# Optimization experiments

Hardware: AMD Instinct MI355X
Metric: run time of the kernel (lower is better)

Reference implementation:

```python
import jax, jax.numpy as jnp
import numpy as np

D_MODEL = 512
NUM_HEADS = 8
D_K = D_MODEL // NUM_HEADS
DIM_FF = 2048
EPS = 1e-5


def layer_norm(x, gamma, beta):
    mu = jnp.mean(x, axis=-1, keepdims=True)
    var = jnp.mean(jnp.square(x - mu), axis=-1, keepdims=True)
    return (x - mu) * jax.lax.rsqrt(var + EPS) * gamma + beta


def setup_inputs() -> dict:
    key = jax.random.key(0)
    ks = jax.random.split(key, 10)
    B, L = 8, 1024
    s = 1.0 / np.sqrt(D_MODEL)
    return {
        "h": jax.random.normal(ks[0], (B, L, D_MODEL), jnp.float32),
        "attn_bias": jax.random.normal(ks[1], (B, NUM_HEADS, L, L), jnp.float32),
        "mask": jnp.ones((B, L), jnp.int32),
        "Wqkv": jax.random.normal(ks[2], (D_MODEL, 3 * D_MODEL), jnp.float32) * s,
        "bqkv": jnp.zeros((3 * D_MODEL,), jnp.float32),
        "Wo": jax.random.normal(ks[3], (D_MODEL, D_MODEL), jnp.float32) * s,
        "bo": jnp.zeros((D_MODEL,), jnp.float32),
        "W1": jax.random.normal(ks[4], (D_MODEL, DIM_FF), jnp.float32) * s,
        "b1": jnp.zeros((DIM_FF,), jnp.float32),
        "W2": jax.random.normal(ks[5], (DIM_FF, D_MODEL), jnp.float32) * (1.0 / np.sqrt(DIM_FF)),
        "b2": jnp.zeros((D_MODEL,), jnp.float32),
        "g1": jnp.ones((D_MODEL,), jnp.float32),
        "be1": jnp.zeros((D_MODEL,), jnp.float32),
        "g2": jnp.ones((D_MODEL,), jnp.float32),
        "be2": jnp.zeros((D_MODEL,), jnp.float32),
    }


def reference(h, attn_bias, mask, Wqkv, bqkv, Wo, bo, W1, b1, W2, b2, g1, be1, g2, be2):
    B, L, D = h.shape
    H, dk = NUM_HEADS, D_K
    qkv = h @ Wqkv + bqkv                      # [B, L, 3D]
    q, k, v = jnp.split(qkv, 3, axis=-1)
    q = q.reshape(B, L, H, dk).transpose(0, 2, 1, 3)  # [B, H, L, dk]
    k = k.reshape(B, L, H, dk).transpose(0, 2, 1, 3)
    v = v.reshape(B, L, H, dk).transpose(0, 2, 1, 3)
    scores = jnp.einsum('bhqd,bhkd->bhqk', q, k) / np.sqrt(dk)
    scores = scores + attn_bias
    scores = jnp.where(mask[:, None, None, :] > 0, scores, -jnp.inf)
    attn = jax.nn.softmax(scores, axis=-1)
    out = jnp.einsum('bhqk,bhkd->bhqd', attn, v)       # [B, H, L, dk]
    out = out.transpose(0, 2, 1, 3).reshape(B, L, D)
    out = out @ Wo + bo
    h = layer_norm(h + out, g1, be1)
    ff = jax.nn.relu(h @ W1 + b1) @ W2 + b2
    h = layer_norm(h + ff, g2, be2)
    return h
```

## Files before the change

kernel.cpp:

```cpp
#include <hip/hip_runtime.h>
#include <hip/hip_bf16.h>
#include <math.h>

#define NUM_HEADS 8
#define SEQ_L 1024
#define EPS 1e-5f
#define LOG2E 1.44269504088896f

typedef __bf16 bf16x8 __attribute__((ext_vector_type(8)));
typedef float f32x4 __attribute__((ext_vector_type(4)));
typedef __hip_bfloat16 bf16;

#define AS1 __attribute__((address_space(1)))
#define AS3 __attribute__((address_space(3)))

__device__ __forceinline__ void gload_lds16(const void* g, void* l) {
    __builtin_amdgcn_global_load_lds((const AS1 unsigned*)g, (AS3 unsigned*)l, 16, 0, 0);
}

__device__ __forceinline__ unsigned short bfb(float x) {
    bf16 b = __float2bfloat16(x);
    return *(unsigned short*)&b;
}

__device__ __forceinline__ int swz(int el, int row) { return el ^ ((row & 7) << 3); }

__global__ __launch_bounds__(256) void prep_kernel(
    const float* __restrict__ h, const float* __restrict__ Wqkv,
    const float* __restrict__ Wo, const float* __restrict__ W1,
    const float* __restrict__ W2,
    bf16* __restrict__ hb, bf16* __restrict__ Wtq, bf16* __restrict__ Wto,
    bf16* __restrict__ Wt1, bf16* __restrict__ Wt2)
{
    const int bid = blockIdx.x;
    const int tid = threadIdx.x;
    if (bid < 2048) {
        const int i = (bid * 256 + tid) * 8;
        const float4 v0 = *(const float4*)&h[i];
        const float4 v1 = *(const float4*)&h[i + 4];
        uint4 w;
        w.x = (unsigned)bfb(v0.x) | ((unsigned)bfb(v0.y) << 16);
        w.y = (unsigned)bfb(v0.z) | ((unsigned)bfb(v0.w) << 16);
        w.z = (unsigned)bfb(v1.x) | ((unsigned)bfb(v1.y) << 16);
        w.w = (unsigned)bfb(v1.z) | ((unsigned)bfb(v1.w) << 16);
        *(uint4*)&hb[i] = w;
        return;
    }
    int r = bid - 2048;
    const float* W; bf16* Wt; int K, N, bx, by;
    if (r < 768)        { W = Wqkv; Wt = Wtq; K = 512;  N = 1536; bx = r % 48; by = r / 48; }
    else if (r < 1024)  { r -= 768;  W = Wo; Wt = Wto; K = 512;  N = 512;  bx = r % 16; by = r / 16; }
    else if (r < 2048)  { r -= 1024; W = W1; Wt = Wt1; K = 512;  N = 2048; bx = r % 64; by = r / 64; }
    else                { r -= 2048; W = W2; Wt = Wt2; K = 2048; N = 512;  bx = r % 16; by = r / 16; }

    __shared__ float t[32][33];
    const int tx = tid & 31, ty = tid >> 5;
    const int n0 = bx * 32, k0 = by * 32;
    #pragma unroll
    for (int q = 0; q < 4; ++q)
        t[ty + 8 * q][tx] = W[(size_t)(k0 + ty + 8 * q) * N + n0 + tx];
    __syncthreads();
    #pragma unroll
    for (int q = 0; q < 4; ++q)
        Wt[(size_t)(n0 + ty + 8 * q) * K + k0 + tx] = __float2bfloat16(t[tx][ty + 8 * q]);
}

__global__ __launch_bounds__(256) void gemm_bf16(
    const bf16* __restrict__ A, const bf16* __restrict__ Bt,
    const float* __restrict__ bias, bf16* __restrict__ Cb,
    int M, int N, int K, int relu)
{
    __shared__ __align__(16) bf16 Abuf[128 * 32];
    __shared__ __align__(16) bf16 Bbuf[128 * 32];
    const int tid = threadIdx.x;
    const int wv = tid >> 6, lane = tid & 63;
    const int row0 = blockIdx.y * 128, col0 = blockIdx.x * 128;
    const int wm = (wv >> 1) * 64, wn = (wv & 1) * 64;
    const int r0 = lane & 15, kb = lane >> 4;

    f32x4 acc[4][4] = {};
    const int arow = lane >> 2;
    const int akoff = (lane & 3) * 8;

    for (int k0 = 0; k0 < K; k0 += 32) {
        #pragma unroll
        for (int s = 0; s < 2; ++s) {
            const int c = 2 * wv + s;
            gload_lds16(&A[(size_t)(row0 + c * 16 + arow) * K + k0 + akoff], &Abuf[c * 512]);
            gload_lds16(&Bt[(size_t)(col0 + c * 16 + arow) * K + k0 + akoff], &Bbuf[c * 512]);
        }
        __syncthreads();

        bf16x8 a[4], b[4];
        #pragma unroll
        for (int i = 0; i < 4; ++i)
            a[i] = *(const bf16x8*)&Abuf[(wm + i * 16 + r0) * 32 + kb * 8];
        #pragma unroll
        for (int j = 0; j < 4; ++j)
            b[j] = *(const bf16x8*)&Bbuf[(wn + j * 16 + r0) * 32 + kb * 8];
        #pragma unroll
        for (int i = 0; i < 4; ++i)
            #pragma unroll
            for (int j = 0; j < 4; ++j)
                acc[i][j] = __builtin_amdgcn_mfma_f32_16x16x32_bf16(a[i], b[j], acc[i][j], 0, 0, 0);
        __syncthreads();
    }

    float bv[4];
    #pragma unroll
    for (int j = 0; j < 4; ++j) bv[j] = bias[col0 + wn + j * 16 + r0];

    #pragma unroll
    for (int i = 0; i < 4; ++i) {
        #pragma unroll
        for (int j = 0; j < 4; ++j) {
            const int col = col0 + wn + j * 16 + r0;
            #pragma unroll
            for (int reg = 0; reg < 4; ++reg) {
                const int row = row0 + wm + i * 16 + kb * 4 + reg;
                float v = acc[i][j][reg] + bv[j];
                if (relu) v = fmaxf(v, 0.f);
                Cb[(size_t)row * N + col] = __float2bfloat16(v);
            }
        }
    }
}

__global__ __launch_bounds__(256) void gemm_qkv(
    const bf16* __restrict__ A, const bf16* __restrict__ Bt,
    const float* __restrict__ bias,
    bf16* __restrict__ Qb, bf16* __restrict__ Kb, bf16* __restrict__ Vtb,
    int M, int N, int K)
{
    __shared__ __align__(16) bf16 Abuf[128 * 32];
    __shared__ __align__(16) bf16 Bbuf[128 * 32];
    const int tid = threadIdx.x;
    const int wv = tid >> 6, lane = tid & 63;
    const int row0 = blockIdx.y * 128, col0 = blockIdx.x * 128;
    const int wm = (wv >> 1) * 64, wn = (wv & 1) * 64;
    const int r0 = lane & 15, kb = lane >> 4;

    f32x4 acc[4][4] = {};
    const int arow = lane >> 2;
    const int akoff = (lane & 3) * 8;

    for (int k0 = 0; k0 < K; k0 += 32) {
        #pragma unroll
        for (int s = 0; s < 2; ++s) {
            const int c = 2 * wv + s;
            gload_lds16(&A[(size_t)(row0 + c * 16 + arow) * K + k0 + akoff], &Abuf[c * 512]);
            gload_lds16(&Bt[(size_t)(col0 + c * 16 + arow) * K + k0 + akoff], &Bbuf[c * 512]);
        }
        __syncthreads();

        bf16x8 a[4], b[4];
        #pragma unroll
        for (int i = 0; i < 4; ++i)
            a[i] = *(const bf16x8*)&Abuf[(wm + i * 16 + r0) * 32 + kb * 8];
        #pragma unroll
        for (int j = 0; j < 4; ++j)
            b[j] = *(const bf16x8*)&Bbuf[(wn + j * 16 + r0) * 32 + kb * 8];
        #pragma unroll
        for (int i = 0; i < 4; ++i)
            #pragma unroll
            for (int j = 0; j < 4; ++j)
                acc[i][j] = __builtin_amdgcn_mfma_f32_16x16x32_bf16(a[i], b[j], acc[i][j], 0, 0, 0);
        __syncthreads();
    }

    #pragma unroll
    for (int i = 0; i < 4; ++i) {
        #pragma unroll
        for (int j = 0; j < 4; ++j) {
            const int col = col0 + wn + j * 16 + r0;
            const float bv = bias[col];
            const int region = col >> 9;
            const int cc = col & 511;
            const int head = cc >> 6, d = cc & 63;
            const int l0 = row0 + wm + i * 16 + kb * 4;
            const int b_ = l0 >> 10, l_ = l0 & 1023;
            if (region == 2) {
                unsigned short pk[4];
                #pragma unroll
                for (int reg = 0; reg < 4; ++reg) pk[reg] = bfb(acc[i][j][reg] + bv);
                *(ushort4*)&Vtb[((size_t)(b_ * NUM_HEADS + head) * 64 + d) * SEQ_L + l_] =
                    make_ushort4(pk[0], pk[1], pk[2], pk[3]);
            } else {
                const float s = (region == 0) ? (0.125f * LOG2E) : 1.0f;
                bf16* dst = (region == 0) ? Qb : Kb;
                #pragma unroll
                for (int reg = 0; reg < 4; ++reg) {
                    dst[((size_t)(b_ * NUM_HEADS + head) * SEQ_L + l_ + reg) * 64 + d] =
                        __float2bfloat16((acc[i][j][reg] + bv) * s);
                }
            }
        }
    }
}

#define KVB 128
__global__ __launch_bounds__(256) void attn_mfma(
    const bf16* __restrict__ Qb, const bf16* __restrict__ Kb,
    const bf16* __restrict__ Vtb, const float* __restrict__ abias,
    const int* __restrict__ mask, bf16* __restrict__ out)
{
    const int bh = blockIdx.y;
    const int b = bh >> 3, h = bh & 7;
    const int q0 = blockIdx.x * 64;
    const int tid = threadIdx.x;
    const int wv = tid >> 6, lane = tid & 63;
    const int ql = lane & 15;
    const int hi = lane >> 4;

    __shared__ __align__(16) bf16 Ks[KVB * 64];
    __shared__ __align__(16) bf16 Vs[64 * KVB];
    __shared__ __align__(16) bf16 Ps[4][16 * KVB];

    const int qrow = q0 + wv * 16 + ql;
    bf16x8 qf[2];
    #pragma unroll
    for (int kk = 0; kk < 2; ++kk)
        qf[kk] = *(const bf16x8*)&Qb[((size_t)bh * SEQ_L + qrow) * 64 + kk * 32 + hi * 8];

    const int skr = tid >> 3;
    const int skc = (tid & 7) * 8;
    const int svr = tid >> 4;
    const int svc = (tid & 15) * 8;

    f32x4 o[4] = {};
    float m = -1e30f, l = 0.f;
    const size_t bias_row = ((size_t)(b * NUM_HEADS + h) * SEQ_L + qrow) * SEQ_L;
    const bf16* Kbase = Kb + (size_t)bh * SEQ_L * 64;
    const bf16* Vbase = Vtb + (size_t)bh * 64 * SEQ_L;
    const int* mbase = mask + b * SEQ_L;

    for (int k0 = 0; k0 < SEQ_L; k0 += KVB) {
        __syncthreads();
        #pragma unroll
        for (int it = 0; it < 4; ++it) {
            const int row = skr + it * 32;
            *(bf16x8*)&Ks[swz(row * 64 + skc, row)] =
                *(const bf16x8*)&Kbase[(size_t)(k0 + row) * 64 + skc];
        }
        #pragma unroll
        for (int it = 0; it < 4; ++it) {
            const int row = svr + it * 16;
            *(bf16x8*)&Vs[swz(row * KVB + svc, row)] =
                *(const bf16x8*)&Vbase[(size_t)row * SEQ_L + k0 + svc];
        }
        __syncthreads();

        f32x4 p[8];
        #pragma unroll
        for (int c = 0; c < 8; ++c) {
            const f32x4 b4 = *(const f32x4*)&abias[bias_row + k0 + c * 16 + hi * 4];
            const int4 m4 = *(const int4*)&mbase[k0 + c * 16 + hi * 4];
            p[c][0] = (m4.x > 0) ? b4[0] * LOG2E : -1e30f;
            p[c][1] = (m4.y > 0) ? b4[1] * LOG2E : -1e30f;
            p[c][2] = (m4.z > 0) ? b4[2] * LOG2E : -1e30f;
            p[c][3] = (m4.w > 0) ? b4[3] * LOG2E : -1e30f;
        }

        __builtin_amdgcn_s_setprio(1);
        #pragma unroll
        for (int c = 0; c < 8; ++c) {
            const int row = c * 16 + ql;
            #pragma unroll
            for (int kk = 0; kk < 2; ++kk) {
                const bf16x8 kf = *(const bf16x8*)&Ks[swz(row * 64 + kk * 32 + hi * 8, row)];
                p[c] = __builtin_amdgcn_mfma_f32_16x16x32_bf16(kf, qf[kk], p[c], 0, 0, 0);
            }
        }
        __builtin_amdgcn_s_setprio(0);

        float mx = p[0][0];
        #pragma unroll
        for (int c = 0; c < 8; ++c)
            #pragma unroll
            for (int reg = 0; reg < 4; ++reg) mx = fmaxf(mx, p[c][reg]);
        mx = fmaxf(mx, __shfl_xor(mx, 16, 64));
        mx = fmaxf(mx, __shfl_xor(mx, 32, 64));

        if (!__all(mx <= m + 11.0f)) {
            const float mnew = fmaxf(m, mx);
            const float scale = __builtin_exp2f(m - mnew);
            m = mnew;
            l *= scale;
            #pragma unroll
            for (int reg = 0; reg < 4; ++reg) {
                const float sc_q = __shfl(scale, (lane & 48) | (hi * 4 + reg), 64);
                #pragma unroll
                for (int c2 = 0; c2 < 4; ++c2) o[c2][reg] *= sc_q;
            }
        }

        float lsum = 0.f;
        #pragma unroll
        for (int c = 0; c < 8; ++c)
            #pragma unroll
            for (int reg = 0; reg < 4; ++reg) {
                const float pv = __builtin_exp2f(p[c][reg] - m);
                p[c][reg] = pv;
                lsum += pv;
            }
        l += lsum;

        #pragma unroll
        for (int c = 0; c < 8; ++c) {
            const int el = ql * KVB + c * 16 + hi * 4;
            uint2 pk;
            pk.x = (unsigned)bfb(p[c][0]) | ((unsigned)bfb(p[c][1]) << 16);
            pk.y = (unsigned)bfb(p[c][2]) | ((unsigned)bfb(p[c][3]) << 16);
            *(uint2*)&Ps[wv][swz(el, ql)] = pk;
        }

        __builtin_amdgcn_s_setprio(1);
        #pragma unroll
        for (int kk = 0; kk < 4; ++kk) {
            const bf16x8 pf = *(const bf16x8*)&Ps[wv][swz(ql * KVB + kk * 32 + hi * 8, ql)];
            #pragma unroll
            for (int c2 = 0; c2 < 4; ++c2) {
                const int vrow = c2 * 16 + ql;
                const bf16x8 vf = *(const bf16x8*)&Vs[swz(vrow * KVB + kk * 32 + hi * 8, vrow)];
                o[c2] = __builtin_amdgcn_mfma_f32_16x16x32_bf16(pf, vf, o[c2], 0, 0, 0);
            }
        }
        __builtin_amdgcn_s_setprio(0);
    }

    l += __shfl_xor(l, 16, 64);
    l += __shfl_xor(l, 32, 64);
    const float invl = (l > 0.f) ? (1.0f / l) : 0.f;
    #pragma unroll
    for (int reg = 0; reg < 4; ++reg) {
        const float inv_q = __shfl(invl, (lane & 48) | (hi * 4 + reg), 64);
        const int row = q0 + wv * 16 + hi * 4 + reg;
        #pragma unroll
        for (int c2 = 0; c2 < 4; ++c2)
            out[((size_t)(b * SEQ_L + row)) * 512 + h * 64 + c2 * 16 + ql] =
                __float2bfloat16(o[c2][reg] * inv_q);
    }
}

__global__ __launch_bounds__(256) void add_ln_to_bf16(
    const float* __restrict__ X, const bf16* __restrict__ Yb,
    const float* __restrict__ gamma, const float* __restrict__ beta,
    bf16* __restrict__ outb)
{
    const int wave = threadIdx.x >> 6;
    const int lane = threadIdx.x & 63;
    const int row = blockIdx.x * 4 + wave;
    const float* xp = X + (size_t)row * 512 + lane * 8;
    const bf16x8 yv = *(const bf16x8*)&Yb[(size_t)row * 512 + lane * 8];

    float v[8];
    const float4 a0 = *(const float4*)xp;
    const float4 a1 = *(const float4*)(xp + 4);
    v[0] = a0.x + (float)yv[0]; v[1] = a0.y + (float)yv[1];
    v[2] = a0.z + (float)yv[2]; v[3] = a0.w + (float)yv[3];
    v[4] = a1.x + (float)yv[4]; v[5] = a1.y + (float)yv[5];
    v[6] = a1.z + (float)yv[6]; v[7] = a1.w + (float)yv[7];

    float s = 0.f, sq = 0.f;
    #pragma unroll
    for (int i = 0; i < 8; ++i) { s += v[i]; sq += v[i] * v[i]; }
    #pragma unroll
    for (int off = 1; off < 64; off <<= 1) {
        s += __shfl_xor(s, off, 64);
        sq += __shfl_xor(sq, off, 64);
    }
    const float mu = s * (1.f / 512.f);
    const float var = sq * (1.f / 512.f) - mu * mu;
    const float rstd = rsqrtf(var + EPS);

    const int c = lane * 8;
    const float4 g0 = *(const float4*)&gamma[c];
    const float4 g1 = *(const float4*)&gamma[c + 4];
    const float4 e0 = *(const float4*)&beta[c];
    const float4 e1 = *(const float4*)&beta[c + 4];
    float r[8];
    r[0] = (v[0] - mu) * rstd * g0.x + e0.x;
    r[1] = (v[1] - mu) * rstd * g0.y + e0.y;
    r[2] = (v[2] - mu) * rstd * g0.z + e0.z;
    r[3] = (v[3] - mu) * rstd * g0.w + e0.w;
    r[4] = (v[4] - mu) * rstd * g1.x + e1.x;
    r[5] = (v[5] - mu) * rstd * g1.y + e1.y;
    r[6] = (v[6] - mu) * rstd * g1.z + e1.z;
    r[7] = (v[7] - mu) * rstd * g1.w + e1.w;

    uint4 w;
    w.x = (unsigned)bfb(r[0]) | ((unsigned)bfb(r[1]) << 16);
    w.y = (unsigned)bfb(r[2]) | ((unsigned)bfb(r[3]) << 16);
    w.z = (unsigned)bfb(r[4]) | ((unsigned)bfb(r[5]) << 16);
    w.w = (unsigned)bfb(r[6]) | ((unsigned)bfb(r[7]) << 16);
    *(uint4*)&outb[(size_t)row * 512 + c] = w;
}

__global__ __launch_bounds__(256) void add_ln_from_bf16(
    const bf16* __restrict__ Xb, const bf16* __restrict__ Yb,
    const float* __restrict__ gamma, const float* __restrict__ beta,
    float* __restrict__ out)
{
    const int wave = threadIdx.x >> 6;
    const int lane = threadIdx.x & 63;
    const int row = blockIdx.x * 4 + wave;
    const bf16x8 xv = *(const bf16x8*)&Xb[(size_t)row * 512 + lane * 8];
    const bf16x8 yv = *(const bf16x8*)&Yb[(size_t)row * 512 + lane * 8];

    float v[8];
    #pragma unroll
    for (int i = 0; i < 8; ++i) v[i] = (float)xv[i] + (float)yv[i];

    float s = 0.f, sq = 0.f;
    #pragma unroll
    for (int i = 0; i < 8; ++i) { s += v[i]; sq += v[i] * v[i]; }
    #pragma unroll
    for (int off = 1; off < 64; off <<= 1) {
        s += __shfl_xor(s, off, 64);
        sq += __shfl_xor(sq, off, 64);
    }
    const float mu = s * (1.f / 512.f);
    const float var = sq * (1.f / 512.f) - mu * mu;
    const float rstd = rsqrtf(var + EPS);

    const int c = lane * 8;
    const float4 g0 = *(const float4*)&gamma[c];
    const float4 g1 = *(const float4*)&gamma[c + 4];
    const float4 e0 = *(const float4*)&beta[c];
    const float4 e1 = *(const float4*)&beta[c + 4];
    float4 r0, r1;
    r0.x = (v[0] - mu) * rstd * g0.x + e0.x;
    r0.y = (v[1] - mu) * rstd * g0.y + e0.y;
    r0.z = (v[2] - mu) * rstd * g0.z + e0.z;
    r0.w = (v[3] - mu) * rstd * g0.w + e0.w;
    r1.x = (v[4] - mu) * rstd * g1.x + e1.x;
    r1.y = (v[5] - mu) * rstd * g1.y + e1.y;
    r1.z = (v[6] - mu) * rstd * g1.z + e1.z;
    r1.w = (v[7] - mu) * rstd * g1.w + e1.w;
    float* op = out + (size_t)row * 512 + c;
    *(float4*)op = r0;
    *(float4*)(op + 4) = r1;
}

extern "C" void kernel_launch(void* const* d_in, const int* in_sizes, int n_in,
                              void* d_out, int out_size, void* d_ws, size_t ws_size,
                              hipStream_t stream)
{
    const float* h    = (const float*)d_in[0];
    const float* ab   = (const float*)d_in[1];
    const int*   mask = (const int*)d_in[2];
    const float* Wqkv = (const float*)d_in[3];
    const float* bqkv = (const float*)d_in[4];
    const float* Wo   = (const float*)d_in[5];
    const float* bo   = (const float*)d_in[6];
    const float* W1   = (const float*)d_in[7];
    const float* b1   = (const float*)d_in[8];
    const float* W2   = (const float*)d_in[9];
    const float* b2   = (const float*)d_in[10];
    const float* g1   = (const float*)d_in[11];
    const float* be1  = (const float*)d_in[12];
    const float* g2   = (const float*)d_in[13];
    const float* be2  = (const float*)d_in[14];
    float* out = (float*)d_out;
    char* ws = (char*)d_ws;

    const int M = 8 * 1024;
    const size_t MB = 1024 * 1024;

    bf16*  hb    = (bf16*)(ws + 0 * MB);
    bf16*  Wtq   = (bf16*)(ws + 8 * MB);
    bf16*  Wto   = (bf16*)(ws + 10 * MB);
    bf16*  Wt1   = (bf16*)(ws + 11 * MB);
    bf16*  Wt2   = (bf16*)(ws + 13 * MB);
    bf16*  Qb    = (bf16*)(ws + 15 * MB);
    bf16*  Kb    = (bf16*)(ws + 23 * MB);
    bf16*  Vtb   = (bf16*)(ws + 31 * MB);
    bf16*  aob   = (bf16*)(ws + 39 * MB);
    bf16*  projb = (bf16*)(ws + 47 * MB);
    bf16*  h1b   = (bf16*)(ws + 55 * MB);
    bf16*  ffb   = (bf16*)(ws + 63 * MB);
    bf16*  f2b   = (bf16*)(ws + 95 * MB);

    prep_kernel<<<dim3(5120), 256, 0, stream>>>(h, Wqkv, Wo, W1, W2, hb, Wtq, Wto, Wt1, Wt2);
    gemm_qkv<<<dim3(1536 / 128, M / 128), 256, 0, stream>>>(hb, Wtq, bqkv, Qb, Kb, Vtb, M, 1536, 512);
    attn_mfma<<<dim3(SEQ_L / 64, 64), 256, 0, stream>>>(Qb, Kb, Vtb, ab, mask, aob);
    gemm_bf16<<<dim3(512 / 128, M / 128), 256, 0, stream>>>(aob, Wto, bo, projb, M, 512, 512, 0);
    add_ln_to_bf16<<<dim3(M / 4), 256, 0, stream>>>(h, projb, g1, be1, h1b);
    gemm_bf16<<<dim3(2048 / 128, M / 128), 256, 0, stream>>>(h1b, Wt1, b1, ffb, M, 2048, 512, 1);
    gemm_bf16<<<dim3(512 / 128, M / 128), 256, 0, stream>>>(ffb, Wt2, b2, f2b, M, 512, 2048, 0);
    add_ln_from_bf16<<<dim3(M / 4), 256, 0, stream>>>(h1b, f2b, g2, be2, out);
}
```

Before: 240.9 us.

## Double-buffer K/V via direct global-to-LDS loads and prefetch bias through LDS

The attention kernel now double-buffers the K and V tiles in LDS and fills them with asynchronous global_load_lds copies, with the pre-swizzled layout computed on the global address side. The next tile's bias and mask are loaded into registers during the current tile's compute, then staged into the P scratch buffer as bf16. This replaces the two full syncthreads per iteration with a single counted-wait barrier, so memory traffic can overlap the MFMA work. In exchange it doubles K/V LDS use, which may lower occupancy, and it rounds the bias to bf16, which reduces precision. The hand-tuned vmcnt wait count has to match the number of outstanding loads exactly.

```diff
diff --git a/kernel.cpp b/kernel.cpp
--- a/kernel.cpp
+++ b/kernel.cpp
@@ -6,6 +6,7 @@
 #define SEQ_L 1024
 #define EPS 1e-5f
 #define LOG2E 1.44269504088896f
+#define KVB 128
 
 typedef __bf16 bf16x8 __attribute__((ext_vector_type(8)));
 typedef float f32x4 __attribute__((ext_vector_type(4)));
@@ -198,7 +199,6 @@
     }
 }
 
-#define KVB 128
 __global__ __launch_bounds__(256) void attn_mfma(
     const bf16* __restrict__ Qb, const bf16* __restrict__ Kb,
     const bf16* __restrict__ Vtb, const float* __restrict__ abias,
@@ -212,54 +212,90 @@
     const int ql = lane & 15;
     const int hi = lane >> 4;
 
-    __shared__ __align__(16) bf16 Ks[KVB * 64];
-    __shared__ __align__(16) bf16 Vs[64 * KVB];
+    __shared__ __align__(16) bf16 Ks[2][KVB * 64];
+    __shared__ __align__(16) bf16 Vs[2][64 * KVB];
     __shared__ __align__(16) bf16 Ps[4][16 * KVB];
 
-    const int qrow = q0 + wv * 16 + ql;
-    bf16x8 qf[2];
-    #pragma unroll
-    for (int kk = 0; kk < 2; ++kk)
-        qf[kk] = *(const bf16x8*)&Qb[((size_t)bh * SEQ_L + qrow) * 64 + kk * 32 + hi * 8];
-
-    const int skr = tid >> 3;
-    const int skc = (tid & 7) * 8;
-    const int svr = tid >> 4;
-    const int svc = (tid & 15) * 8;
-
-    f32x4 o[4] = {};
-    float m = -1e30f, l = 0.f;
-    const size_t bias_row = ((size_t)(b * NUM_HEADS + h) * SEQ_L + qrow) * SEQ_L;
     const bf16* Kbase = Kb + (size_t)bh * SEQ_L * 64;
     const bf16* Vbase = Vtb + (size_t)bh * 64 * SEQ_L;
     const int* mbase = mask + b * SEQ_L;
 
-    for (int k0 = 0; k0 < SEQ_L; k0 += KVB) {
-        __syncthreads();
+    auto stageKV = [&](int buf, int k0) {
         #pragma unroll
         for (int it = 0; it < 4; ++it) {
-            const int row = skr + it * 32;
-            *(bf16x8*)&Ks[swz(row * 64 + skc, row)] =
-                *(const bf16x8*)&Kbase[(size_t)(k0 + row) * 64 + skc];
+            const int row = wv * 32 + it * 8 + (lane >> 3);
+            const int gp = (lane & 7) ^ (row & 7);
+            gload_lds16(&Kbase[(size_t)(k0 + row) * 64 + gp * 8],
+                        &Ks[buf][(wv * 32 + it * 8) * 64]);
         }
         #pragma unroll
         for (int it = 0; it < 4; ++it) {
-            const int row = svr + it * 16;
-            *(bf16x8*)&Vs[swz(row * KVB + svc, row)] =
-                *(const bf16x8*)&Vbase[(size_t)row * SEQ_L + k0 + svc];
-        }
-        __syncthreads();
-
+            const int row = wv * 16 + it * 4 + (lane >> 4);
+            const int g = lane & 15;
+            const int gp = (g & 8) | ((g & 7) ^ (row & 7));
+            gload_lds16(&Vbase[(size_t)row * SEQ_L + k0 + gp * 8],
+                        &Vs[buf][(wv * 16 + it * 4) * KVB]);
+        }
+    };
+
+    const int brow2 = lane >> 5;
+    const int bcolq = lane & 31;
+    const size_t bias_base = ((size_t)(b * NUM_HEADS + h) * SEQ_L + q0 + wv * 16) * SEQ_L;
+    f32x4 breg[8];
+    int4 mreg4;
+    auto loadBias = [&](int k0) {
+        mreg4 = *(const int4*)&mbase[k0 + bcolq * 4];
+        #pragma unroll
+        for (int s = 0; s < 8; ++s)
+            breg[s] = *(const f32x4*)&abias[bias_base + (size_t)(s * 2 + brow2) * SEQ_L + k0 + bcolq * 4];
+    };
+    const unsigned short NEGBIG = bfb(-1e30f);
+    auto writeBias = [&]() {
+        #pragma unroll
+        for (int s = 0; s < 8; ++s) {
+            const int row = s * 2 + brow2;
+            const unsigned short w0 = (mreg4.x > 0) ? bfb(breg[s][0]) : NEGBIG;
+            const unsigned short w1 = (mreg4.y > 0) ? bfb(breg[s][1]) : NEGBIG;
+            const unsigned short w2 = (mreg4.z > 0) ? bfb(breg[s][2]) : NEGBIG;
+            const unsigned short w3 = (mreg4.w > 0) ? bfb(breg[s][3]) : NEGBIG;
+            uint2 pk;
+            pk.x = (unsigned)w0 | ((unsigned)w1 << 16);
+            pk.y = (unsigned)w2 | ((unsigned)w3 << 16);
+            const int el = (row * KVB + bcolq * 4) ^ ((row & 7) << 2);
+            *(uint2*)&Ps[wv][el] = pk;
+        }
+    };
+
+    stageKV(0, 0);
+    const int qrow = q0 + wv * 16 + ql;
+    bf16x8 qf[2];
+    #pragma unroll
+    for (int kk = 0; kk < 2; ++kk)
+        qf[kk] = *(const bf16x8*)&Qb[((size_t)bh * SEQ_L + qrow) * 64 + kk * 32 + hi * 8];
+    loadBias(0);
+    writeBias();
+    __builtin_amdgcn_sched_barrier(0);
+    __builtin_amdgcn_s_barrier();
+    __builtin_amdgcn_sched_barrier(0);
+    stageKV(1, KVB);
+
+    f32x4 o[4] = {};
+    float m = -1e30f, l = 0.f;
+    int cur = 0;
+
+    for (int t = 0; t < 8; ++t) {
         f32x4 p[8];
         #pragma unroll
         for (int c = 0; c < 8; ++c) {
-            const f32x4 b4 = *(const f32x4*)&abias[bias_row + k0 + c * 16 + hi * 4];
-            const int4 m4 = *(const int4*)&mbase[k0 + c * 16 + hi * 4];
-            p[c][0] = (m4.x > 0) ? b4[0] * LOG2E : -1e30f;
-            p[c][1] = (m4.y > 0) ? b4[1] * LOG2E : -1e30f;
-            p[c][2] = (m4.z > 0) ? b4[2] * LOG2E : -1e30f;
-            p[c][3] = (m4.w > 0) ? b4[3] * LOG2E : -1e30f;
-        }
+            const int el = (ql * KVB + c * 16 + hi * 4) ^ ((ql & 7) << 2);
+            const uint2 pk = *(const uint2*)&Ps[wv][el];
+            p[c][0] = __uint_as_float((pk.x & 0xffffu) << 16) * LOG2E;
+            p[c][1] = __uint_as_float(pk.x & 0xffff0000u) * LOG2E;
+            p[c][2] = __uint_as_float((pk.y & 0xffffu) << 16) * LOG2E;
+            p[c][3] = __uint_as_float(pk.y & 0xffff0000u) * LOG2E;
+        }
+
+        if (t < 7) loadBias((t + 1) * KVB);
 
         __builtin_amdgcn_s_setprio(1);
         #pragma unroll
@@ -267,7 +303,7 @@
             const int row = c * 16 + ql;
             #pragma unroll
             for (int kk = 0; kk < 2; ++kk) {
-                const bf16x8 kf = *(const bf16x8*)&Ks[swz(row * 64 + kk * 32 + hi * 8, row)];
+                const bf16x8 kf = *(const bf16x8*)&Ks[cur][swz(row * 64 + kk * 32 + hi * 8, row)];
                 p[c] = __builtin_amdgcn_mfma_f32_16x16x32_bf16(kf, qf[kk], p[c], 0, 0, 0);
             }
         }
@@ -321,11 +357,21 @@
             #pragma unroll
             for (int c2 = 0; c2 < 4; ++c2) {
                 const int vrow = c2 * 16 + ql;
-                const bf16x8 vf = *(const bf16x8*)&Vs[swz(vrow * KVB + kk * 32 + hi * 8, vrow)];
+                const bf16x8 vf = *(const bf16x8*)&Vs[cur][swz(vrow * KVB + kk * 32 + hi * 8, vrow)];
                 o[c2] = __builtin_amdgcn_mfma_f32_16x16x32_bf16(pf, vf, o[c2], 0, 0, 0);
             }
         }
         __builtin_amdgcn_s_setprio(0);
+
+        if (t < 7) {
+            __builtin_amdgcn_sched_barrier(0);
+            asm volatile("s_waitcnt vmcnt(9)" ::: "memory");
+            __builtin_amdgcn_s_barrier();
+            __builtin_amdgcn_sched_barrier(0);
+            if (t < 6) stageKV(cur, (t + 2) * KVB);
+            writeBias();
+            cur ^= 1;
+        }
     }
 
     l += __shfl_xor(l, 16, 64);
```

After: 240.5 us. Within noise of the previous version (-0.2%).

## Prefetch attention bias/mask, stage K/V via direct-to-LDS loads, swap grid order

Applied to the files above, without the earlier changes.

The attention kernel now loads K and V tiles with global_load_lds directly into LDS, applying the swizzle on the global side. It prefetches the next tile's bias and mask into registers while the current tile's MFMAs run, so those global-load latencies overlap with compute. All GEMM and attention launches swap grid x/y so consecutive blocks walk the M (or batch-head) dimension, which changes L2 reuse of weights and K/V. The cost is higher register pressure from the prefetched bias and mask, plus no overlap of the K/V staging itself, since it still sits between barriers.

```diff
diff --git a/kernel.cpp b/kernel.cpp
--- a/kernel.cpp
+++ b/kernel.cpp
@@ -6,6 +6,7 @@
 #define SEQ_L 1024
 #define EPS 1e-5f
 #define LOG2E 1.44269504088896f
+#define KVB 128
 
 typedef __bf16 bf16x8 __attribute__((ext_vector_type(8)));
 typedef float f32x4 __attribute__((ext_vector_type(4)));
@@ -74,7 +75,7 @@
     __shared__ __align__(16) bf16 Bbuf[128 * 32];
     const int tid = threadIdx.x;
     const int wv = tid >> 6, lane = tid & 63;
-    const int row0 = blockIdx.y * 128, col0 = blockIdx.x * 128;
+    const int row0 = blockIdx.x * 128, col0 = blockIdx.y * 128;
     const int wm = (wv >> 1) * 64, wn = (wv & 1) * 64;
     const int r0 = lane & 15, kb = lane >> 4;
 
@@ -136,7 +137,7 @@
     __shared__ __align__(16) bf16 Bbuf[128 * 32];
     const int tid = threadIdx.x;
     const int wv = tid >> 6, lane = tid & 63;
-    const int row0 = blockIdx.y * 128, col0 = blockIdx.x * 128;
+    const int row0 = blockIdx.x * 128, col0 = blockIdx.y * 128;
     const int wm = (wv >> 1) * 64, wn = (wv & 1) * 64;
     const int r0 = lane & 15, kb = lane >> 4;
 
@@ -198,15 +199,14 @@
     }
 }
 
-#define KVB 128
 __global__ __launch_bounds__(256) void attn_mfma(
     const bf16* __restrict__ Qb, const bf16* __restrict__ Kb,
     const bf16* __restrict__ Vtb, const float* __restrict__ abias,
     const int* __restrict__ mask, bf16* __restrict__ out)
 {
-    const int bh = blockIdx.y;
+    const int bh = blockIdx.x;
     const int b = bh >> 3, h = bh & 7;
-    const int q0 = blockIdx.x * 64;
+    const int q0 = blockIdx.y * 64;
     const int tid = threadIdx.x;
     const int wv = tid >> 6, lane = tid & 63;
     const int ql = lane & 15;
@@ -216,50 +216,71 @@
     __shared__ __align__(16) bf16 Vs[64 * KVB];
     __shared__ __align__(16) bf16 Ps[4][16 * KVB];
 
-    const int qrow = q0 + wv * 16 + ql;
-    bf16x8 qf[2];
-    #pragma unroll
-    for (int kk = 0; kk < 2; ++kk)
-        qf[kk] = *(const bf16x8*)&Qb[((size_t)bh * SEQ_L + qrow) * 64 + kk * 32 + hi * 8];
-
-    const int skr = tid >> 3;
-    const int skc = (tid & 7) * 8;
-    const int svr = tid >> 4;
-    const int svc = (tid & 15) * 8;
-
-    f32x4 o[4] = {};
-    float m = -1e30f, l = 0.f;
-    const size_t bias_row = ((size_t)(b * NUM_HEADS + h) * SEQ_L + qrow) * SEQ_L;
     const bf16* Kbase = Kb + (size_t)bh * SEQ_L * 64;
     const bf16* Vbase = Vtb + (size_t)bh * 64 * SEQ_L;
     const int* mbase = mask + b * SEQ_L;
 
-    for (int k0 = 0; k0 < SEQ_L; k0 += KVB) {
-        __syncthreads();
+    auto stageKV = [&](int k0) {
         #pragma unroll
         for (int it = 0; it < 4; ++it) {
-            const int row = skr + it * 32;
-            *(bf16x8*)&Ks[swz(row * 64 + skc, row)] =
-                *(const bf16x8*)&Kbase[(size_t)(k0 + row) * 64 + skc];
+            const int row = wv * 32 + it * 8 + (lane >> 3);
+            const int gp = (lane & 7) ^ (row & 7);
+            gload_lds16(&Kbase[(size_t)(k0 + row) * 64 + gp * 8],
+                        &Ks[(wv * 32 + it * 8) * 64]);
         }
         #pragma unroll
         for (int it = 0; it < 4; ++it) {
-            const int row = svr + it * 16;
-            *(bf16x8*)&Vs[swz(row * KVB + svc, row)] =
-                *(const bf16x8*)&Vbase[(size_t)row * SEQ_L + k0 + svc];
-        }
-        __syncthreads();
-
+            const int row = wv * 16 + it * 4 + (lane >> 4);
+            const int g = lane & 15;
+            const int gp = (g & 8) | ((g & 7) ^ (row & 7));
+            gload_lds16(&Vbase[(size_t)row * SEQ_L + k0 + gp * 8],
+                        &Vs[(wv * 16 + it * 4) * KVB]);
+        }
+    };
+
+    const int qrow = q0 + wv * 16 + ql;
+    bf16x8 qf[2];
+    #pragma unroll
+    for (int kk = 0; kk < 2; ++kk)
+        qf[kk] = *(const bf16x8*)&Qb[((size_t)bh * SEQ_L + qrow) * 64 + kk * 32 + hi * 8];
+
+    const size_t bias_row = ((size_t)(b * NUM_HEADS + h) * SEQ_L + qrow) * SEQ_L;
+
+    f32x4 breg[8];
+    int4 mreg[2];
+    auto loadBias = [&](int k0) {
+        #pragma unroll
+        for (int c = 0; c < 8; ++c)
+            breg[c] = *(const f32x4*)&abias[bias_row + k0 + c * 16 + hi * 4];
+        mreg[0] = *(const int4*)&mbase[k0 + (hi * 4)];
+        mreg[1] = *(const int4*)&mbase[k0 + 64 + (hi * 4)];
+    };
+    int4 mfr[8];
+    auto loadMask = [&](int k0) {
+        #pragma unroll
+        for (int c = 0; c < 8; ++c)
+            mfr[c] = *(const int4*)&mbase[k0 + c * 16 + hi * 4];
+    };
+
+    f32x4 o[4] = {};
+    float m = -1e30f, l = 0.f;
+
+    stageKV(0);
+    loadBias(0);
+    loadMask(0);
+    __syncthreads();
+
+    for (int t = 0; t < 8; ++t) {
         f32x4 p[8];
         #pragma unroll
         for (int c = 0; c < 8; ++c) {
-            const f32x4 b4 = *(const f32x4*)&abias[bias_row + k0 + c * 16 + hi * 4];
-            const int4 m4 = *(const int4*)&mbase[k0 + c * 16 + hi * 4];
-            p[c][0] = (m4.x > 0) ? b4[0] * LOG2E : -1e30f;
-            p[c][1] = (m4.y > 0) ? b4[1] * LOG2E : -1e30f;
-            p[c][2] = (m4.z > 0) ? b4[2] * LOG2E : -1e30f;
-            p[c][3] = (m4.w > 0) ? b4[3] * LOG2E : -1e30f;
-        }
+            p[c][0] = (mfr[c].x > 0) ? breg[c][0] * LOG2E : -1e30f;
+            p[c][1] = (mfr[c].y > 0) ? breg[c][1] * LOG2E : -1e30f;
+            p[c][2] = (mfr[c].z > 0) ? breg[c][2] * LOG2E : -1e30f;
+            p[c][3] = (mfr[c].w > 0) ? breg[c][3] * LOG2E : -1e30f;
+        }
+
+        if (t < 7) { loadBias((t + 1) * KVB); loadMask((t + 1) * KVB); }
 
         __builtin_amdgcn_s_setprio(1);
         #pragma unroll
@@ -326,6 +347,12 @@
             }
         }
         __builtin_amdgcn_s_setprio(0);
+
+        if (t < 7) {
+            __syncthreads();
+            stageKV((t + 1) * KVB);
+            __syncthreads();
+        }
     }
 
     l += __shfl_xor(l, 16, 64);
@@ -482,11 +509,11 @@
     bf16*  f2b   = (bf16*)(ws + 95 * MB);
 
     prep_kernel<<<dim3(5120), 256, 0, stream>>>(h, Wqkv, Wo, W1, W2, hb, Wtq, Wto, Wt1, Wt2);
-    gemm_qkv<<<dim3(1536 / 128, M / 128), 256, 0, stream>>>(hb, Wtq, bqkv, Qb, Kb, Vtb, M, 1536, 512);
-    attn_mfma<<<dim3(SEQ_L / 64, 64), 256, 0, stream>>>(Qb, Kb, Vtb, ab, mask, aob);
-    gemm_bf16<<<dim3(512 / 128, M / 128), 256, 0, stream>>>(aob, Wto, bo, projb, M, 512, 512, 0);
+    gemm_qkv<<<dim3(M / 128, 1536 / 128), 256, 0, stream>>>(hb, Wtq, bqkv, Qb, Kb, Vtb, M, 1536, 512);
+    attn_mfma<<<dim3(64, SEQ_L / 64), 256, 0, stream>>>(Qb, Kb, Vtb, ab, mask, aob);
+    gemm_bf16<<<dim3(M / 128, 512 / 128), 256, 0, stream>>>(aob, Wto, bo, projb, M, 512, 512, 0);
     add_ln_to_bf16<<<dim3(M / 4), 256, 0, stream>>>(h, projb, g1, be1, h1b);
-    gemm_bf16<<<dim3(2048 / 128, M / 128), 256, 0, stream>>>(h1b, Wt1, b1, ffb, M, 2048, 512, 1);
-    gemm_bf16<<<dim3(512 / 128, M / 128), 256, 0, stream>>>(ffb, Wt2, b2, f2b, M, 512, 2048, 0);
+    gemm_bf16<<<dim3(M / 128, 2048 / 128), 256, 0, stream>>>(h1b, Wt1, b1, ffb, M, 2048, 512, 1);
+    gemm_bf16<<<dim3(M / 128, 512 / 128), 256, 0, stream>>>(ffb, Wt2, b2, f2b, M, 512, 2048, 0);
     add_ln_from_bf16<<<dim3(M / 4), 256, 0, stream>>>(h1b, f2b, g2, be2, out);
 }
```

Result: faster. 229.8 us (-4.6%).
